# Kernel optimization log

Hardware: AMD Instinct MI355X
Metric: run time of the kernel (lower is better)

## Reference

```python
import jax, jax.numpy as jnp
import numpy as np

MAX_DIST = 5
D_PE = 16
NUM_ENTITIES = 50000
NUM_EDGES = 800000
NUM_ANCHOR_TRIPLES = 32
MAX_SOURCES = 2 * NUM_ANCHOR_TRIPLES  # upper bound on unique anchor entities


def setup_inputs() -> dict:
    key = jax.random.key(0)
    k1, k2, k3, k4 = jax.random.split(key, 4)
    h_ids = jax.random.randint(k1, (NUM_EDGES,), 0, NUM_ENTITIES)
    t_ids = jax.random.randint(k2, (NUM_EDGES,), 0, NUM_ENTITIES)
    anchor_triple_indices = jax.random.randint(k3, (NUM_ANCHOR_TRIPLES,), 0, NUM_EDGES)
    dist_embed = jax.random.normal(k4, (MAX_DIST + 1, D_PE), dtype=jnp.float32)
    return {
        "h_ids": h_ids,
        "t_ids": t_ids,
        "anchor_triple_indices": anchor_triple_indices,
        "num_entities": NUM_ENTITIES,
        "dist_embed": dist_embed,
    }


def _bfs_mean_counts(h_ids, t_ids, anchor_triple_indices, num_entities):
    """Returns [num_entities, MAX_DIST+1] mean one-hot distance counts over anchors."""
    # unique anchor entities, padded with -1 to a static size (torch.unique equivalent)
    anchor_ents = jnp.concatenate([h_ids[anchor_triple_indices], t_ids[anchor_triple_indices]])
    sources = jnp.unique(anchor_ents, size=MAX_SOURCES, fill_value=-1)  # [K], sorted
    valid = sources >= 0                                                # [K]
    src = jnp.where(valid, sources, 0)
    K = src.shape[0]
    col = jnp.arange(K)

    # symmetric adjacency as edge list (duplicates are harmless: only >0 is tested)
    edge_src = jnp.concatenate([h_ids, t_ids])  # [2E]
    edge_dst = jnp.concatenate([t_ids, h_ids])  # [2E]

    frontier = jnp.zeros((num_entities, K), jnp.float32).at[src, col].set(1.0)
    visited = jnp.zeros((num_entities, K), bool).at[src, col].set(True)
    dist = jnp.full((num_entities, K), MAX_DIST, jnp.int32).at[src, col].set(0)

    for depth in range(1, MAX_DIST + 1):  # fixed small hop count
        # sparse adj @ frontier == scatter-add of gathered frontier rows
        new_frontier = jax.ops.segment_sum(frontier[edge_src], edge_dst, num_segments=num_entities)
        newly = (new_frontier > 0) & ~visited
        dist = jnp.where(newly, depth, dist)
        visited = visited | newly
        frontier = newly.astype(jnp.float32)

    # masked mean over valid anchor sources, expressed as distance-count histogram
    w = valid.astype(jnp.float32)
    n_valid = jnp.maximum(w.sum(), 1.0)
    onehot = jax.nn.one_hot(dist, MAX_DIST + 1, dtype=jnp.float32)  # [N, K, D+1]
    counts = jnp.einsum('nkd,k->nd', onehot, w) / n_valid           # [N, D+1]
    return counts


def reference(h_ids, t_ids, anchor_triple_indices, num_entities, dist_embed):
    counts = _bfs_mean_counts(h_ids, t_ids, anchor_triple_indices, num_entities)
    # mean over sources of embed(dist) == counts @ embedding table
    return counts @ dist_embed  # [num_entities, d_pe]
```

## Files before the change

### kernel.cpp

```cpp
#include <hip/hip_runtime.h>
#include <hip/hip_bf16.h>

typedef unsigned long long u64;
typedef unsigned int u32;
typedef unsigned short u16;

#define MAXD 5
#define BSH  6
#define BN   64
#define PAD  16
#define NW   128
#define NTH  256
#define CAPG 4096


__global__ void zero_kernel(u32* __restrict__ a, int na, u32* __restrict__ b, int nb) {
    int stride = gridDim.x * blockDim.x;
    int i = blockIdx.x * blockDim.x + threadIdx.x;
    for (int k = i; k < na; k += stride) a[k] = 0u;
    for (int k = i; k < nb; k += stride) b[k] = 0u;
}

__global__ void setup_sources(const int* __restrict__ h, const int* __restrict__ t,
                              const int* __restrict__ anchor, int A,
                              u64* __restrict__ F0, u32* __restrict__ srcPack,
                              int* __restrict__ nvalid) {
    int tid = threadIdx.x;
    int K = 2 * A;
    int a_ = (tid < K) ? anchor[(tid < A) ? tid : (tid - A)] : 0;
    int my = (tid < K) ? ((tid < A) ? h[a_] : t[a_]) : -1;
    bool uniq = (tid < K);
    for (int j = 0; j < 64; ++j) {
        int o = __shfl(my, j, 64);
        if (j < tid && o == my) uniq = false;
    }
    u64 mask = __ballot(uniq);
    if (tid == 0) *nvalid = (int)__popcll(mask);
    if (uniq) F0[my] = 1ull << tid;
    srcPack[tid] = uniq ? (((u32)my << BSH) | (u32)tid) : 0xFFFFFFFFu;
}

__global__ void scatter_kernel(const int* __restrict__ h, const int* __restrict__ t,
                               int E, u32* __restrict__ cursorpad,
                               u32* __restrict__ recs, int NB) {
    extern __shared__ u32 sh[];
    u32* lh = sh;
    u32* base = sh + NB;
    int tid = threadIdx.x;
    for (int i = tid; i < NB; i += NTH) lh[i] = 0u;
    __syncthreads();
    int stride = gridDim.x * NTH;
    int t0 = blockIdx.x * NTH + tid;
    for (int e = t0; e < E; e += stride) {
        u32 uu = (u32)h[e], vv = (u32)t[e];
        atomicAdd(&lh[vv >> BSH], 1u);
        atomicAdd(&lh[uu >> BSH], 1u);
    }
    __syncthreads();
    for (int i = tid; i < NB; i += NTH) {
        u32 c = lh[i];
        base[i] = c ? atomicAdd(&cursorpad[i * PAD], c) : 0u;
    }
    __syncthreads();
    for (int i = tid; i < NB; i += NTH) lh[i] = 0u;
    __syncthreads();
    for (int e = t0; e < E; e += stride) {
        u32 uu = (u32)h[e], vv = (u32)t[e];
        u32 b1 = vv >> BSH;
        u32 r1 = base[b1] + atomicAdd(&lh[b1], 1u);
        if (r1 < CAPG) recs[b1 * CAPG + r1] = (uu << BSH) | (vv & (BN - 1));
        u32 b2 = uu >> BSH;
        u32 r2 = base[b2] + atomicAdd(&lh[b2], 1u);
        if (r2 < CAPG) recs[b2 * CAPG + r2] = (vv << BSH) | (uu & (BN - 1));
    }
}

__global__ __launch_bounds__(NTH) void level1_sort(
    const u32* __restrict__ recs, const u32* __restrict__ cursorpad,
    const u32* __restrict__ srcPack, const u64* __restrict__ F0,
    u64* __restrict__ F1, u64* __restrict__ V, u64* __restrict__ CNT,
    u16* __restrict__ srec, u32* __restrict__ laneOff, int N) {
    __shared__ u32 recsL[CAPG];
    __shared__ u32 laneCnt[BN];
    __shared__ u32 laneCur[BN];
    __shared__ u64 NF[BN];
    __shared__ u32 srcL[64];
    int b = blockIdx.x, tid = threadIdx.x;
    u32 o0 = (u32)b * CAPG;
    u32 cnt = min(cursorpad[b * PAD], (u32)CAPG);
    if (tid < BN) { laneCnt[tid] = 0u; NF[tid] = 0ull; }
    if (tid < 64) srcL[tid] = srcPack[tid];
    __syncthreads();
    for (u32 r = tid; r < cnt; r += NTH) {
        u32 rec = recs[o0 + r];
        recsL[r] = rec;
        atomicAdd(&laneCnt[rec & (BN - 1)], 1u);
    }
    __syncthreads();
    if (tid < 64) {
        u32 v = laneCnt[tid];
        u32 p = v;
        for (int d = 1; d < 64; d <<= 1) {
            u32 x = __shfl_up(p, d, 64);
            if (tid >= d) p += x;
        }
        u32 excl = p - v;
        laneCur[tid] = excl;
        laneOff[b * (BN + 1) + tid] = o0 + excl;
        if (tid == 63) laneOff[b * (BN + 1) + 64] = o0 + p;
    }
    __syncthreads();
    for (u32 r = tid; r < cnt; r += NTH) {
        u32 rec = recsL[r];
        u32 lane = rec & (BN - 1);
        u32 src = rec >> BSH;
        u32 pos = atomicAdd(&laneCur[lane], 1u);
        srec[o0 + pos] = (u16)src;
        u64 f = F0[src];
        if (f) atomicOr(&NF[lane], f);
    }
    __syncthreads();
    if (tid < BN) {
        int n = b * BN + tid;
        if (n < N) {
            u64 srcbit = 0ull;
            for (int k = 0; k < 64; ++k) {
                u32 p = srcL[k];
                if (p != 0xFFFFFFFFu && (int)(p >> BSH) == n)
                    srcbit |= 1ull << (p & (BN - 1));
            }
            u64 newly = NF[tid] & ~srcbit;
            V[n] = srcbit | newly;
            F1[n] = newly;
            CNT[n] = (srcbit ? 1ull : 0ull) | ((u64)__popcll(newly) << 8);
        }
    }
}

__global__ __launch_bounds__(NTH) void level_q(
    const u16* __restrict__ srec, const u32* __restrict__ laneOff,
    const u64* __restrict__ Fin, u64* __restrict__ Fout,
    u64* __restrict__ V, u64* __restrict__ CNT, int N, int shift) {
    __shared__ u32 loL[BN + 1];
    int b = blockIdx.x, tid = threadIdx.x;
    if (tid <= BN) loL[tid] = laneOff[b * (BN + 1) + tid];
    __syncthreads();
    int nl = tid >> 2, q = tid & 3;
    u32 r = loL[nl] + q, r1 = loL[nl + 1];
    u64 reg = 0ull;
    for (; r + 4 < r1; r += 8) {
        u32 s0 = srec[r], s1 = srec[r + 4];
        reg |= Fin[s0] | Fin[s1];
    }
    if (r < r1) reg |= Fin[srec[r]];
    reg |= __shfl_xor(reg, 1, 64);
    reg |= __shfl_xor(reg, 2, 64);
    if (q == 0) {
        int n = b * BN + nl;
        if (n < N) {
            u64 vis = V[n];
            u64 newly = reg & ~vis;
            Fout[n] = newly;
            if (newly) {
                V[n] = vis | newly;
                CNT[n] += (u64)__popcll(newly) << shift;
            }
        }
    }
}

__global__ __launch_bounds__(NTH) void level4_fin(
    const u16* __restrict__ srec, const u32* __restrict__ laneOff,
    const u64* __restrict__ Fin, const u64* __restrict__ V,
    const u64* __restrict__ CNT, const int* __restrict__ nvalid,
    const float* __restrict__ embed, float* __restrict__ out, int N) {
    __shared__ u32 loL[BN + 1];
    int b = blockIdx.x, tid = threadIdx.x;
    if (tid <= BN) loL[tid] = laneOff[b * (BN + 1) + tid];
    __syncthreads();
    int nl = tid >> 2, q = tid & 3;
    u32 r = loL[nl] + q, r1 = loL[nl + 1];
    u64 reg = 0ull;
    for (; r + 4 < r1; r += 8) {
        u32 s0 = srec[r], s1 = srec[r + 4];
        reg |= Fin[s0] | Fin[s1];
    }
    if (r < r1) reg |= Fin[srec[r]];
    reg |= __shfl_xor(reg, 1, 64);
    reg |= __shfl_xor(reg, 2, 64);
    int n = b * BN + nl;
    if (n >= N) return;
    u64 vis = V[n];
    int c4 = __popcll(reg & ~vis);
    u64 c = CNT[n];
    int nv = *nvalid;
    float inv = 1.0f / (float)(nv > 0 ? nv : 1);
    float cd[MAXD + 1];
    int total = c4;
#pragma unroll
    for (int d = 0; d < 4; ++d) {
        int x = (int)((c >> (8 * d)) & 0xffull);
        total += x;
        cd[d] = (float)x;
    }
    cd[4] = (float)c4;
    cd[5] = (float)(nv - total);

    const float4* e4 = (const float4*)embed;
    float4 acc = {0.f, 0.f, 0.f, 0.f};
#pragma unroll
    for (int d = 0; d <= MAXD; ++d) {
        float4 e = e4[d * 4 + q];
        acc.x += cd[d] * e.x; acc.y += cd[d] * e.y;
        acc.z += cd[d] * e.z; acc.w += cd[d] * e.w;
    }
    acc.x *= inv; acc.y *= inv; acc.z *= inv; acc.w *= inv;
    ((float4*)(out + (size_t)n * 16))[q] = acc;
}

extern "C" void kernel_launch(void* const* d_in, const int* in_sizes, int n_in,
                              void* d_out, int out_size, void* d_ws, size_t ws_size,
                              hipStream_t stream) {
    const int*   h      = (const int*)d_in[0];
    const int*   t      = (const int*)d_in[1];
    const int*   anchor = (const int*)d_in[2];
    const float* embed  = (const float*)d_in[4];
    float*       out    = (float*)d_out;

    int E = in_sizes[0];
    int A = in_sizes[2];
    int D = in_sizes[4] / (MAXD + 1);
    int N = out_size / D;
    int NB = (N + BN - 1) >> BSH;
    (void)D;

    u64* F0  = (u64*)d_ws;
    u64* F1  = F0 + N;
    u64* V   = F1 + N;
    u64* CNT = V + N;
    u32* cursorpad = (u32*)(CNT + N);
    u32* srcPack   = cursorpad + (size_t)NB * PAD;
    int* nvalid    = (int*)(srcPack + 64);
    u32* laneOff   = (u32*)(nvalid + 1);
    u32* recs      = laneOff + (size_t)NB * (BN + 1);
    u16* srec      = (u16*)(recs + (size_t)NB * CAPG);

    zero_kernel<<<256, NTH, 0, stream>>>((u32*)F0, 2 * N, cursorpad, NB * PAD);
    setup_sources<<<1, 64, 0, stream>>>(h, t, anchor, A, F0, srcPack, nvalid);
    scatter_kernel<<<NW, NTH, 2 * NB * sizeof(u32), stream>>>(h, t, E, cursorpad, recs, NB);

    level1_sort<<<NB, NTH, 0, stream>>>(recs, cursorpad, srcPack, F0,
                                        F1, V, CNT, srec, laneOff, N);
    level_q<<<NB, NTH, 0, stream>>>(srec, laneOff, F1, F0, V, CNT, N, 16);
    level_q<<<NB, NTH, 0, stream>>>(srec, laneOff, F0, F1, V, CNT, N, 24);
    level4_fin<<<NB, NTH, 0, stream>>>(srec, laneOff, F1, V, CNT, nvalid,
                                       embed, out, N);
}
```

Baseline: 147.2 us.

## Pad per-node edge lists to quads and fuse source setup into scatter

Each node's neighbour list in srec is padded to a multiple of four with a sentinel index that points into zeroed frontier padding. This lets each of the four threads per node scan a contiguous quarter with 4-way unrolled loads, replacing the strided interleaved loop. The single-block source-setup kernel is folded into block 0 of the scatter kernel to save a launch, the scatter grid is doubled, and the per-bucket record capacity is reduced. The risks are a little extra sentinel work per node and a tighter bucket capacity that could truncate heavily loaded buckets.

```diff
diff --git a/kernel.cpp b/kernel.cpp
--- a/kernel.cpp
+++ b/kernel.cpp
@@ -9,9 +9,10 @@
 #define BSH  6
 #define BN   64
 #define PAD  16
-#define NW   128
+#define NW   256
 #define NTH  256
-#define CAPG 4096
+#define CAPG 2816
+#define NPADF 65536
 
 
 __global__ void zero_kernel(u32* __restrict__ a, int na, u32* __restrict__ b, int nb) {
@@ -21,32 +22,32 @@
     for (int k = i; k < nb; k += stride) b[k] = 0u;
 }
 
-__global__ void setup_sources(const int* __restrict__ h, const int* __restrict__ t,
+__global__ void scatter_setup(const int* __restrict__ h, const int* __restrict__ t,
+                              int E, u32* __restrict__ cursorpad,
+                              u32* __restrict__ recs, int NB,
                               const int* __restrict__ anchor, int A,
                               u64* __restrict__ F0, u32* __restrict__ srcPack,
                               int* __restrict__ nvalid) {
-    int tid = threadIdx.x;
-    int K = 2 * A;
-    int a_ = (tid < K) ? anchor[(tid < A) ? tid : (tid - A)] : 0;
-    int my = (tid < K) ? ((tid < A) ? h[a_] : t[a_]) : -1;
-    bool uniq = (tid < K);
-    for (int j = 0; j < 64; ++j) {
-        int o = __shfl(my, j, 64);
-        if (j < tid && o == my) uniq = false;
-    }
-    u64 mask = __ballot(uniq);
-    if (tid == 0) *nvalid = (int)__popcll(mask);
-    if (uniq) F0[my] = 1ull << tid;
-    srcPack[tid] = uniq ? (((u32)my << BSH) | (u32)tid) : 0xFFFFFFFFu;
-}
-
-__global__ void scatter_kernel(const int* __restrict__ h, const int* __restrict__ t,
-                               int E, u32* __restrict__ cursorpad,
-                               u32* __restrict__ recs, int NB) {
     extern __shared__ u32 sh[];
     u32* lh = sh;
     u32* base = sh + NB;
     int tid = threadIdx.x;
+
+    if (blockIdx.x == 0 && tid < 64) {
+        int K = 2 * A;
+        int a_ = (tid < K) ? anchor[(tid < A) ? tid : (tid - A)] : 0;
+        int my = (tid < K) ? ((tid < A) ? h[a_] : t[a_]) : -1;
+        bool uniq = (tid < K);
+        for (int j = 0; j < 64; ++j) {
+            int o = __shfl(my, j, 64);
+            if (j < tid && o == my) uniq = false;
+        }
+        u64 mask = __ballot(uniq);
+        if (tid == 0) *nvalid = (int)__popcll(mask);
+        if (uniq) F0[my] = 1ull << tid;
+        srcPack[tid] = uniq ? (((u32)my << BSH) | (u32)tid) : 0xFFFFFFFFu;
+    }
+
     for (int i = tid; i < NB; i += NTH) lh[i] = 0u;
     __syncthreads();
     int stride = gridDim.x * NTH;
@@ -83,11 +84,12 @@
     __shared__ u32 recsL[CAPG];
     __shared__ u32 laneCnt[BN];
     __shared__ u32 laneCur[BN];
+    __shared__ u32 lanePend[BN];
     __shared__ u64 NF[BN];
     __shared__ u32 srcL[64];
     int b = blockIdx.x, tid = threadIdx.x;
     u32 o0 = (u32)b * CAPG;
-    u32 cnt = min(cursorpad[b * PAD], (u32)CAPG);
+    u32 cnt = min(cursorpad[b * PAD], (u32)(CAPG - 4 * BN));
     if (tid < BN) { laneCnt[tid] = 0u; NF[tid] = 0ull; }
     if (tid < 64) srcL[tid] = srcPack[tid];
     __syncthreads();
@@ -99,13 +101,15 @@
     __syncthreads();
     if (tid < 64) {
         u32 v = laneCnt[tid];
-        u32 p = v;
+        u32 pv = (v + 3u) & ~3u;
+        u32 p = pv;
         for (int d = 1; d < 64; d <<= 1) {
             u32 x = __shfl_up(p, d, 64);
             if (tid >= d) p += x;
         }
-        u32 excl = p - v;
+        u32 excl = p - pv;
         laneCur[tid] = excl;
+        lanePend[tid] = excl + pv;
         laneOff[b * (BN + 1) + tid] = o0 + excl;
         if (tid == 63) laneOff[b * (BN + 1) + 64] = o0 + p;
     }
@@ -120,6 +124,10 @@
         if (f) atomicOr(&NF[lane], f);
     }
     __syncthreads();
+    if (tid < 64) {
+        for (u32 p = laneCur[tid]; p < lanePend[tid]; ++p)
+            srec[o0 + p] = (u16)0xFFFF;
+    }
     if (tid < BN) {
         int n = b * BN + tid;
         if (n < N) {
@@ -146,13 +154,17 @@
     if (tid <= BN) loL[tid] = laneOff[b * (BN + 1) + tid];
     __syncthreads();
     int nl = tid >> 2, q = tid & 3;
-    u32 r = loL[nl] + q, r1 = loL[nl + 1];
+    u32 lo = loL[nl];
+    u32 quarter = (loL[nl + 1] - lo) >> 2;
+    u32 base = lo + q * quarter;
     u64 reg = 0ull;
-    for (; r + 4 < r1; r += 8) {
-        u32 s0 = srec[r], s1 = srec[r + 4];
-        reg |= Fin[s0] | Fin[s1];
-    }
-    if (r < r1) reg |= Fin[srec[r]];
+    u32 i = 0;
+    for (; i + 4 <= quarter; i += 4) {
+        u32 s0 = srec[base + i],     s1 = srec[base + i + 1];
+        u32 s2 = srec[base + i + 2], s3 = srec[base + i + 3];
+        reg |= Fin[s0] | Fin[s1] | Fin[s2] | Fin[s3];
+    }
+    for (; i < quarter; ++i) reg |= Fin[srec[base + i]];
     reg |= __shfl_xor(reg, 1, 64);
     reg |= __shfl_xor(reg, 2, 64);
     if (q == 0) {
@@ -179,13 +191,17 @@
     if (tid <= BN) loL[tid] = laneOff[b * (BN + 1) + tid];
     __syncthreads();
     int nl = tid >> 2, q = tid & 3;
-    u32 r = loL[nl] + q, r1 = loL[nl + 1];
+    u32 lo = loL[nl];
+    u32 quarter = (loL[nl + 1] - lo) >> 2;
+    u32 base = lo + q * quarter;
     u64 reg = 0ull;
-    for (; r + 4 < r1; r += 8) {
-        u32 s0 = srec[r], s1 = srec[r + 4];
-        reg |= Fin[s0] | Fin[s1];
-    }
-    if (r < r1) reg |= Fin[srec[r]];
+    u32 i = 0;
+    for (; i + 4 <= quarter; i += 4) {
+        u32 s0 = srec[base + i],     s1 = srec[base + i + 1];
+        u32 s2 = srec[base + i + 2], s3 = srec[base + i + 3];
+        reg |= Fin[s0] | Fin[s1] | Fin[s2] | Fin[s3];
+    }
+    for (; i < quarter; ++i) reg |= Fin[srec[base + i]];
     reg |= __shfl_xor(reg, 1, 64);
     reg |= __shfl_xor(reg, 2, 64);
     int n = b * BN + nl;
@@ -235,8 +251,8 @@
     (void)D;
 
     u64* F0  = (u64*)d_ws;
-    u64* F1  = F0 + N;
-    u64* V   = F1 + N;
+    u64* F1  = F0 + NPADF;
+    u64* V   = F1 + NPADF;
     u64* CNT = V + N;
     u32* cursorpad = (u32*)(CNT + N);
     u32* srcPack   = cursorpad + (size_t)NB * PAD;
@@ -245,9 +261,9 @@
     u32* recs      = laneOff + (size_t)NB * (BN + 1);
     u16* srec      = (u16*)(recs + (size_t)NB * CAPG);
 
-    zero_kernel<<<256, NTH, 0, stream>>>((u32*)F0, 2 * N, cursorpad, NB * PAD);
-    setup_sources<<<1, 64, 0, stream>>>(h, t, anchor, A, F0, srcPack, nvalid);
-    scatter_kernel<<<NW, NTH, 2 * NB * sizeof(u32), stream>>>(h, t, E, cursorpad, recs, NB);
+    zero_kernel<<<256, NTH, 0, stream>>>((u32*)F0, 2 * NPADF * 2, cursorpad, NB * PAD);
+    scatter_setup<<<NW, NTH, 2 * NB * sizeof(u32), stream>>>(
+        h, t, E, cursorpad, recs, NB, anchor, A, F0, srcPack, nvalid);
 
     level1_sort<<<NB, NTH, 0, stream>>>(recs, cursorpad, srcPack, F0,
                                         F1, V, CNT, srec, laneOff, N);
```

Result: faster. 144.1 us (-2.1%).

## Fuse source setup and level-1 BFS into scatter, drop per-lane sort

Applied to the files above, without the earlier changes.

Source deduplication moves into the scatter kernel, which builds a shared-memory hash of anchor entities and computes the level-1 frontier directly with global atomicOr while bucketing edges. The per-node lane sort and 16-bit source array go away. Later levels scan the unsorted bucket records and merge frontier bits with shared-memory atomicOr per lane, and one fewer level kernel is launched. Zeroing becomes a hipMemsetAsync, scatter uses more workgroups, and the bucket capacity shrinks. This trades sorted per-node gathers for shared atomics and adds global 64-bit atomics plus a hash probe per edge during scatter. The smaller capacity raises the risk of overflowing buckets.

```diff
diff --git a/kernel.cpp b/kernel.cpp
--- a/kernel.cpp
+++ b/kernel.cpp
@@ -3,52 +3,66 @@
 
 typedef unsigned long long u64;
 typedef unsigned int u32;
-typedef unsigned short u16;
 
 #define MAXD 5
 #define BSH  6
 #define BN   64
 #define PAD  16
-#define NW   128
+#define NW   256
 #define NTH  256
-#define CAPG 4096
-
-
-__global__ void zero_kernel(u32* __restrict__ a, int na, u32* __restrict__ b, int nb) {
-    int stride = gridDim.x * blockDim.x;
-    int i = blockIdx.x * blockDim.x + threadIdx.x;
-    for (int k = i; k < na; k += stride) a[k] = 0u;
-    for (int k = i; k < nb; k += stride) b[k] = 0u;
-}
-
-__global__ void setup_sources(const int* __restrict__ h, const int* __restrict__ t,
+#define CAPG 2816
+#define HEMPTY 0xFFFFFFFFu
+
+
+__global__ void scatter_setup(const int* __restrict__ h, const int* __restrict__ t,
+                              int E, u32* __restrict__ cursorpad,
+                              u32* __restrict__ recs, int NB,
                               const int* __restrict__ anchor, int A,
-                              u64* __restrict__ F0, u32* __restrict__ srcPack,
+                              u64* __restrict__ NFg, u32* __restrict__ srcPack,
                               int* __restrict__ nvalid) {
+    extern __shared__ u32 sh[];
+    u32* lh    = sh;
+    u32* base  = sh + NB;
+    u32* hsKey = sh + 2 * NB;
+    u32* hsBit = hsKey + 128;
     int tid = threadIdx.x;
-    int K = 2 * A;
-    int a_ = (tid < K) ? anchor[(tid < A) ? tid : (tid - A)] : 0;
-    int my = (tid < K) ? ((tid < A) ? h[a_] : t[a_]) : -1;
-    bool uniq = (tid < K);
-    for (int j = 0; j < 64; ++j) {
-        int o = __shfl(my, j, 64);
-        if (j < tid && o == my) uniq = false;
-    }
-    u64 mask = __ballot(uniq);
-    if (tid == 0) *nvalid = (int)__popcll(mask);
-    if (uniq) F0[my] = 1ull << tid;
-    srcPack[tid] = uniq ? (((u32)my << BSH) | (u32)tid) : 0xFFFFFFFFu;
-}
-
-__global__ void scatter_kernel(const int* __restrict__ h, const int* __restrict__ t,
-                               int E, u32* __restrict__ cursorpad,
-                               u32* __restrict__ recs, int NB) {
-    extern __shared__ u32 sh[];
-    u32* lh = sh;
-    u32* base = sh + NB;
-    int tid = threadIdx.x;
+
     for (int i = tid; i < NB; i += NTH) lh[i] = 0u;
-    __syncthreads();
+    if (tid < 128) hsKey[tid] = HEMPTY;
+    __syncthreads();
+
+    if (tid < 64) {
+        int K = 2 * A;
+        int a_ = (tid < K) ? anchor[(tid < A) ? tid : (tid - A)] : 0;
+        int my = (tid < K) ? ((tid < A) ? h[a_] : t[a_]) : -1;
+        bool uniq = (tid < K);
+        for (int j = 0; j < 64; ++j) {
+            int o = __shfl(my, j, 64);
+            if (j < tid && o == my) uniq = false;
+        }
+        u64 mask = __ballot(uniq);
+        if (blockIdx.x == 0 && tid == 0) *nvalid = (int)__popcll(mask);
+        if (uniq) {
+            u32 slot = ((u32)my * 2654435761u) >> 25;
+            while (atomicCAS(&hsKey[slot], HEMPTY, (u32)my) != HEMPTY)
+                slot = (slot + 1) & 127u;
+            hsBit[slot] = (u32)tid;
+        }
+        if (blockIdx.x == 0)
+            srcPack[tid] = uniq ? (((u32)my << BSH) | (u32)tid) : HEMPTY;
+    }
+    __syncthreads();
+
+    auto srcMask = [&](u32 src) -> u64 {
+        u32 slot = (src * 2654435761u) >> 25;
+        while (true) {
+            u32 k = hsKey[slot];
+            if (k == src) return 1ull << hsBit[slot];
+            if (k == HEMPTY) return 0ull;
+            slot = (slot + 1) & 127u;
+        }
+    };
+
     int stride = gridDim.x * NTH;
     int t0 = blockIdx.x * NTH + tid;
     for (int e = t0; e < E; e += stride) {
@@ -72,52 +86,42 @@
         u32 b2 = uu >> BSH;
         u32 r2 = base[b2] + atomicAdd(&lh[b2], 1u);
         if (r2 < CAPG) recs[b2 * CAPG + r2] = (vv << BSH) | (uu & (BN - 1));
-    }
-}
-
-__global__ __launch_bounds__(NTH) void level1_sort(
+        if (uu != vv) {
+            u64 m1 = srcMask(uu);
+            if (m1) atomicOr(&NFg[vv], m1);
+            u64 m2 = srcMask(vv);
+            if (m2) atomicOr(&NFg[uu], m2);
+        }
+    }
+}
+
+__global__ __launch_bounds__(NTH) void level12(
     const u32* __restrict__ recs, const u32* __restrict__ cursorpad,
-    const u32* __restrict__ srcPack, const u64* __restrict__ F0,
-    u64* __restrict__ F1, u64* __restrict__ V, u64* __restrict__ CNT,
-    u16* __restrict__ srec, u32* __restrict__ laneOff, int N) {
-    __shared__ u32 recsL[CAPG];
-    __shared__ u32 laneCnt[BN];
-    __shared__ u32 laneCur[BN];
+    const u32* __restrict__ srcPack, const u64* __restrict__ NFg,
+    u64* __restrict__ F2, u64* __restrict__ V, u64* __restrict__ CNT, int N) {
     __shared__ u64 NF[BN];
     __shared__ u32 srcL[64];
     int b = blockIdx.x, tid = threadIdx.x;
     u32 o0 = (u32)b * CAPG;
     u32 cnt = min(cursorpad[b * PAD], (u32)CAPG);
-    if (tid < BN) { laneCnt[tid] = 0u; NF[tid] = 0ull; }
+    if (tid < BN) NF[tid] = 0ull;
     if (tid < 64) srcL[tid] = srcPack[tid];
     __syncthreads();
-    for (u32 r = tid; r < cnt; r += NTH) {
-        u32 rec = recs[o0 + r];
-        recsL[r] = rec;
-        atomicAdd(&laneCnt[rec & (BN - 1)], 1u);
-    }
-    __syncthreads();
-    if (tid < 64) {
-        u32 v = laneCnt[tid];
-        u32 p = v;
-        for (int d = 1; d < 64; d <<= 1) {
-            u32 x = __shfl_up(p, d, 64);
-            if (tid >= d) p += x;
-        }
-        u32 excl = p - v;
-        laneCur[tid] = excl;
-        laneOff[b * (BN + 1) + tid] = o0 + excl;
-        if (tid == 63) laneOff[b * (BN + 1) + 64] = o0 + p;
-    }
-    __syncthreads();
-    for (u32 r = tid; r < cnt; r += NTH) {
-        u32 rec = recsL[r];
-        u32 lane = rec & (BN - 1);
-        u32 src = rec >> BSH;
-        u32 pos = atomicAdd(&laneCur[lane], 1u);
-        srec[o0 + pos] = (u16)src;
-        u64 f = F0[src];
-        if (f) atomicOr(&NF[lane], f);
+    u32 r = tid;
+    for (; r + 3u * NTH < cnt; r += 4u * NTH) {
+        u32 c0 = recs[o0 + r],           c1 = recs[o0 + r + NTH];
+        u32 c2 = recs[o0 + r + 2 * NTH], c3 = recs[o0 + r + 3 * NTH];
+        u64 f0 = NFg[c0 >> BSH], f1 = NFg[c1 >> BSH];
+        u64 f2 = NFg[c2 >> BSH], f3 = NFg[c3 >> BSH];
+        if (f0) atomicOr(&NF[c0 & (BN - 1)], f0);
+        if (f1) atomicOr(&NF[c1 & (BN - 1)], f1);
+        if (f2) atomicOr(&NF[c2 & (BN - 1)], f2);
+        if (f3) atomicOr(&NF[c3 & (BN - 1)], f3);
+    }
+    for (; r < cnt; r += NTH) {
+        u32 c0 = recs[o0 + r];
+        u64 f0 = NFg[c0 >> BSH];
+        if (f0) atomicOr(&NF[c0 & (BN - 1)], f0);
     }
     __syncthreads();
     if (tid < BN) {
@@ -126,72 +130,95 @@
             u64 srcbit = 0ull;
             for (int k = 0; k < 64; ++k) {
                 u32 p = srcL[k];
-                if (p != 0xFFFFFFFFu && (int)(p >> BSH) == n)
+                if (p != HEMPTY && (int)(p >> BSH) == n)
                     srcbit |= 1ull << (p & (BN - 1));
             }
-            u64 newly = NF[tid] & ~srcbit;
-            V[n] = srcbit | newly;
-            F1[n] = newly;
-            CNT[n] = (srcbit ? 1ull : 0ull) | ((u64)__popcll(newly) << 8);
-        }
-    }
-}
-
-__global__ __launch_bounds__(NTH) void level_q(
-    const u16* __restrict__ srec, const u32* __restrict__ laneOff,
+            u64 nf1 = NFg[n];
+            u64 v1 = srcbit | nf1;
+            u64 newly2 = NF[tid] & ~v1;
+            V[n] = v1 | newly2;
+            F2[n] = newly2;
+            CNT[n] = (srcbit ? 1ull : 0ull)
+                   | ((u64)__popcll(nf1) << 8)
+                   | ((u64)__popcll(newly2) << 16);
+        }
+    }
+}
+
+__global__ __launch_bounds__(NTH) void level3(
+    const u32* __restrict__ recs, const u32* __restrict__ cursorpad,
     const u64* __restrict__ Fin, u64* __restrict__ Fout,
-    u64* __restrict__ V, u64* __restrict__ CNT, int N, int shift) {
-    __shared__ u32 loL[BN + 1];
+    u64* __restrict__ V, u64* __restrict__ CNT, int N) {
+    __shared__ u64 NF[BN];
     int b = blockIdx.x, tid = threadIdx.x;
-    if (tid <= BN) loL[tid] = laneOff[b * (BN + 1) + tid];
-    __syncthreads();
-    int nl = tid >> 2, q = tid & 3;
-    u32 r = loL[nl] + q, r1 = loL[nl + 1];
-    u64 reg = 0ull;
-    for (; r + 4 < r1; r += 8) {
-        u32 s0 = srec[r], s1 = srec[r + 4];
-        reg |= Fin[s0] | Fin[s1];
-    }
-    if (r < r1) reg |= Fin[srec[r]];
-    reg |= __shfl_xor(reg, 1, 64);
-    reg |= __shfl_xor(reg, 2, 64);
-    if (q == 0) {
-        int n = b * BN + nl;
+    u32 o0 = (u32)b * CAPG;
+    u32 cnt = min(cursorpad[b * PAD], (u32)CAPG);
+    if (tid < BN) NF[tid] = 0ull;
+    __syncthreads();
+    u32 r = tid;
+    for (; r + 3u * NTH < cnt; r += 4u * NTH) {
+        u32 c0 = recs[o0 + r],           c1 = recs[o0 + r + NTH];
+        u32 c2 = recs[o0 + r + 2 * NTH], c3 = recs[o0 + r + 3 * NTH];
+        u64 f0 = Fin[c0 >> BSH], f1 = Fin[c1 >> BSH];
+        u64 f2 = Fin[c2 >> BSH], f3 = Fin[c3 >> BSH];
+        if (f0) atomicOr(&NF[c0 & (BN - 1)], f0);
+        if (f1) atomicOr(&NF[c1 & (BN - 1)], f1);
+        if (f2) atomicOr(&NF[c2 & (BN - 1)], f2);
+        if (f3) atomicOr(&NF[c3 & (BN - 1)], f3);
+    }
+    for (; r < cnt; r += NTH) {
+        u32 c0 = recs[o0 + r];
+        u64 f0 = Fin[c0 >> BSH];
+        if (f0) atomicOr(&NF[c0 & (BN - 1)], f0);
+    }
+    __syncthreads();
+    if (tid < BN) {
+        int n = b * BN + tid;
         if (n < N) {
             u64 vis = V[n];
-            u64 newly = reg & ~vis;
+            u64 newly = NF[tid] & ~vis;
             Fout[n] = newly;
             if (newly) {
                 V[n] = vis | newly;
-                CNT[n] += (u64)__popcll(newly) << shift;
+                CNT[n] += (u64)__popcll(newly) << 24;
             }
         }
     }
 }
 
 __global__ __launch_bounds__(NTH) void level4_fin(
-    const u16* __restrict__ srec, const u32* __restrict__ laneOff,
+    const u32* __restrict__ recs, const u32* __restrict__ cursorpad,
     const u64* __restrict__ Fin, const u64* __restrict__ V,
     const u64* __restrict__ CNT, const int* __restrict__ nvalid,
     const float* __restrict__ embed, float* __restrict__ out, int N) {
-    __shared__ u32 loL[BN + 1];
+    __shared__ u64 NF[BN];
     int b = blockIdx.x, tid = threadIdx.x;
-    if (tid <= BN) loL[tid] = laneOff[b * (BN + 1) + tid];
+    u32 o0 = (u32)b * CAPG;
+    u32 cnt = min(cursorpad[b * PAD], (u32)CAPG);
+    if (tid < BN) NF[tid] = 0ull;
+    __syncthreads();
+    u32 r = tid;
+    for (; r + 3u * NTH < cnt; r += 4u * NTH) {
+        u32 c0 = recs[o0 + r],           c1 = recs[o0 + r + NTH];
+        u32 c2 = recs[o0 + r + 2 * NTH], c3 = recs[o0 + r + 3 * NTH];
+        u64 f0 = Fin[c0 >> BSH], f1 = Fin[c1 >> BSH];
+        u64 f2 = Fin[c2 >> BSH], f3 = Fin[c3 >> BSH];
+        if (f0) atomicOr(&NF[c0 & (BN - 1)], f0);
+        if (f1) atomicOr(&NF[c1 & (BN - 1)], f1);
+        if (f2) atomicOr(&NF[c2 & (BN - 1)], f2);
+        if (f3) atomicOr(&NF[c3 & (BN - 1)], f3);
+    }
+    for (; r < cnt; r += NTH) {
+        u32 c0 = recs[o0 + r];
+        u64 f0 = Fin[c0 >> BSH];
+        if (f0) atomicOr(&NF[c0 & (BN - 1)], f0);
+    }
     __syncthreads();
     int nl = tid >> 2, q = tid & 3;
-    u32 r = loL[nl] + q, r1 = loL[nl + 1];
-    u64 reg = 0ull;
-    for (; r + 4 < r1; r += 8) {
-        u32 s0 = srec[r], s1 = srec[r + 4];
-        reg |= Fin[s0] | Fin[s1];
-    }
-    if (r < r1) reg |= Fin[srec[r]];
-    reg |= __shfl_xor(reg, 1, 64);
-    reg |= __shfl_xor(reg, 2, 64);
     int n = b * BN + nl;
     if (n >= N) return;
     u64 vis = V[n];
-    int c4 = __popcll(reg & ~vis);
+    int c4 = __popcll(NF[nl] & ~vis);
     u64 c = CNT[n];
     int nv = *nvalid;
     float inv = 1.0f / (float)(nv > 0 ? nv : 1);
@@ -234,25 +261,23 @@
     int NB = (N + BN - 1) >> BSH;
     (void)D;
 
-    u64* F0  = (u64*)d_ws;
-    u64* F1  = F0 + N;
-    u64* V   = F1 + N;
+    u32* cursorpad = (u32*)d_ws;
+    u64* NFg = (u64*)(cursorpad + (size_t)NB * PAD);
+    u64* V   = NFg + N;
     u64* CNT = V + N;
-    u32* cursorpad = (u32*)(CNT + N);
-    u32* srcPack   = cursorpad + (size_t)NB * PAD;
-    int* nvalid    = (int*)(srcPack + 64);
-    u32* laneOff   = (u32*)(nvalid + 1);
-    u32* recs      = laneOff + (size_t)NB * (BN + 1);
-    u16* srec      = (u16*)(recs + (size_t)NB * CAPG);
-
-    zero_kernel<<<256, NTH, 0, stream>>>((u32*)F0, 2 * N, cursorpad, NB * PAD);
-    setup_sources<<<1, 64, 0, stream>>>(h, t, anchor, A, F0, srcPack, nvalid);
-    scatter_kernel<<<NW, NTH, 2 * NB * sizeof(u32), stream>>>(h, t, E, cursorpad, recs, NB);
-
-    level1_sort<<<NB, NTH, 0, stream>>>(recs, cursorpad, srcPack, F0,
-                                        F1, V, CNT, srec, laneOff, N);
-    level_q<<<NB, NTH, 0, stream>>>(srec, laneOff, F1, F0, V, CNT, N, 16);
-    level_q<<<NB, NTH, 0, stream>>>(srec, laneOff, F0, F1, V, CNT, N, 24);
-    level4_fin<<<NB, NTH, 0, stream>>>(srec, laneOff, F1, V, CNT, nvalid,
+    u64* F2  = CNT + N;
+    u64* F3  = F2 + N;
+    u32* srcPack = (u32*)(F3 + N);
+    int* nvalid  = (int*)(srcPack + 64);
+    u32* recs    = (u32*)(nvalid + 1);
+
+    hipMemsetAsync(d_ws, 0, (size_t)NB * PAD * 4 + (size_t)N * 8, stream);
+
+    scatter_setup<<<NW, NTH, (2 * NB + 256) * sizeof(u32), stream>>>(
+        h, t, E, cursorpad, recs, NB, anchor, A, NFg, srcPack, nvalid);
+
+    level12<<<NB, NTH, 0, stream>>>(recs, cursorpad, srcPack, NFg, F2, V, CNT, N);
+    level3<<<NB, NTH, 0, stream>>>(recs, cursorpad, F2, F3, V, CNT, N);
+    level4_fin<<<NB, NTH, 0, stream>>>(recs, cursorpad, F3, V, CNT, nvalid,
                                        embed, out, N);
 }
```

New measurement: 151.4 us. +2.9%, slower.
